# Kernel optimization log

Hardware: AMD Instinct MI355X
Metric: run time of the kernel (lower is better)

The kernel has to match this reference:

```python
import jax, jax.numpy as jnp
import numpy as np

B = 65536
IN = 64
H = 16
PF = 64


def _linear_params(key, out_dim, in_dim):
    k1, k2 = jax.random.split(key)
    bound = 1.0 / np.sqrt(in_dim)
    W = jax.random.uniform(k1, (out_dim, in_dim), jnp.float32, -bound, bound)
    b = jax.random.uniform(k2, (out_dim,), jnp.float32, -bound, bound)
    return W, b


def setup_inputs() -> dict:
    key = jax.random.key(0)
    ks = jax.random.split(key, 20)
    inp = {}
    for i, name in enumerate(['a', 'v', 'l', 'p_a', 'p_v', 'p_l', 'mean']):
        inp[name] = jax.random.normal(ks[i], (B, IN), jnp.float32)
    inp['Wa'], inp['ba'] = _linear_params(ks[7], H, IN)
    inp['Wv'], inp['bv'] = _linear_params(ks[8], H, IN)
    inp['Wl'], inp['bl'] = _linear_params(ks[9], H, IN)
    inp['Wap'], inp['bap'] = _linear_params(ks[10], H, IN)
    inp['Wvp'], inp['bvp'] = _linear_params(ks[11], H, IN)
    inp['Wlp'], inp['blp'] = _linear_params(ks[12], H, IN)
    inp['Wf1'], inp['bf1'] = _linear_params(ks[13], PF, H ** 3 // 16)
    inp['Wfp1'], inp['bfp1'] = _linear_params(ks[14], PF, H ** 3 // 16)
    inp['Wng'], inp['bng'] = _linear_params(ks[15], 64, 128)
    inp['rm1'] = jnp.zeros((128,), jnp.float32)  # normGate2 running_mean buffers (eval mode)
    inp['rm2'] = jnp.zeros((128,), jnp.float32)
    return inp


def _maxpool2(x):
    # 2x2 stride-2 max pool over the last two dims of [B, Hd, Wd]
    b, hd, wd = x.shape
    return x.reshape(b, hd // 2, 2, wd // 2, 2).max(axis=(2, 4))


def _trimodal_fusion(x_h, y_h, z_h):
    # outer product [B,H,H] -> pool -> [B,H*H//4,1] bmm [B,1,H] -> pool -> flatten
    f = x_h[:, :, None] * y_h[:, None, :]            # [B,16,16]
    f = _maxpool2(f)                                 # [B,8,8]
    f = f.reshape(-1, H * H // 4, 1) * z_h[:, None, :]  # [B,64,16]
    f = _maxpool2(f)                                 # [B,32,8]
    return f.reshape(x_h.shape[0], -1)               # [B,256]


def _norm_gate(x, running_mean):
    # eval-mode normGate2: y = x * sigmoid(|x - running_mean|)
    return x * jax.nn.sigmoid(jnp.abs(x - running_mean))


def reference(a, v, l, p_a, p_v, p_l, mean,
              Wa, ba, Wv, bv, Wl, bl, Wap, bap, Wvp, bvp, Wlp, blp,
              Wf1, bf1, Wfp1, bfp1, Wng, bng, rm1, rm2):
    a_h = jax.nn.sigmoid(a @ Wa.T + ba)
    v_h = jax.nn.sigmoid(v @ Wv.T + bv)
    l_h = jax.nn.sigmoid(l @ Wl.T + bl)
    fusion_1 = jax.nn.leaky_relu(_trimodal_fusion(a_h, v_h, l_h) @ Wf1.T + bf1)

    pa_h = jax.nn.sigmoid(p_a @ Wap.T + bap)
    pv_h = jax.nn.sigmoid(p_v @ Wvp.T + bvp)
    pl_h = jax.nn.sigmoid(p_l @ Wlp.T + blp)
    fusion_2 = jax.nn.leaky_relu(_trimodal_fusion(pa_h, pv_h, pl_h) @ Wfp1.T + bfp1)

    out = _norm_gate(jnp.concatenate([fusion_2, mean], axis=1), rm1)   # [B,128]
    out = out @ Wng.T + bng                                            # [B,64]
    out = _norm_gate(jnp.concatenate([out, fusion_1], axis=1), rm2)    # [B,128]
    return out
```

## Files before the change

### kernel.cpp

```cpp
#include <hip/hip_runtime.h>
#include <hip/hip_bf16.h>


typedef __attribute__((ext_vector_type(8))) short short8;
typedef __attribute__((ext_vector_type(4))) float f32x4;

#define MFMA16(A, B, C) __builtin_amdgcn_mfma_f32_16x16x32_bf16((A), (B), (C), 0, 0, 0)

__device__ __forceinline__ float fast_sigmoid(float x) {
    return __builtin_amdgcn_rcpf(1.0f + __expf(-x));
}
__device__ __forceinline__ float gate(float x, float rm) {
    return x * fast_sigmoid(fabsf(x - rm));
}
__device__ __forceinline__ float lrelu(float x) {
    return x >= 0.0f ? x : 0.01f * x;
}
__device__ __forceinline__ short f2bf(float f) {
    union { float f; unsigned u; } x; x.f = f;
    unsigned r = (x.u + 0x7FFF + ((x.u >> 16) & 1)) >> 16;
    return (short)r;
}
__device__ __forceinline__ short8 pack8(const float* xs) {
    union { short8 s; __hip_bfloat162 h[4]; } u;
    #pragma unroll
    for (int i = 0; i < 4; ++i) {
        float2 t; t.x = xs[2 * i]; t.y = xs[2 * i + 1];
        u.h[i] = __float22bfloat162_rn(t);
    }
    return u.s;
}
__device__ __forceinline__ f32x4 pmax_xor(f32x4 v, int mask) {
    f32x4 r;
    #pragma unroll
    for (int i = 0; i < 4; ++i) r[i] = fmaxf(v[i], __shfl_xor(v[i], mask, 64));
    return r;
}

__device__ __forceinline__ void proj_mfma2(const float* __restrict__ xbase,
                                           const short8* __restrict__ wfr,
                                           const float* __restrict__ bias,
                                           int lane, f32x4& h0, f32x4& h1) {
    const int m = lane & 15, quad = lane >> 4;
    f32x4 a0; a0[0] = a0[1] = a0[2] = a0[3] = 0.0f;
    f32x4 a1 = a0;
    #pragma unroll
    for (int t = 0; t < 2; ++t) {
        const float4* p0 = (const float4*)(xbase + m * 64 + t * 32 + quad * 8);
        const float4* p1 = (const float4*)(xbase + (16 + m) * 64 + t * 32 + quad * 8);
        float4 u0 = p0[0], u1 = p0[1];
        float4 w0 = p1[0], w1 = p1[1];
        const short8 frag = wfr[t * 64 + lane];
        float xs0[8] = {u0.x, u0.y, u0.z, u0.w, u1.x, u1.y, u1.z, u1.w};
        float xs1[8] = {w0.x, w0.y, w0.z, w0.w, w1.x, w1.y, w1.z, w1.w};
        a0 = MFMA16(pack8(xs0), frag, a0);
        a1 = MFMA16(pack8(xs1), frag, a1);
    }
    const float bn = bias[m];
    #pragma unroll
    for (int r = 0; r < 4; ++r) {
        h0[r] = fast_sigmoid(a0[r] + bn);
        h1[r] = fast_sigmoid(a1[r] + bn);
    }
}

__device__ __forceinline__ void stage_pools(f32x4 hx, f32x4 hy, f32x4 hz, int lane,
                                            float* __restrict__ sX,
                                            float* __restrict__ sY,
                                            float* __restrict__ sZ) {
    const int quad = lane >> 4, ln = lane & 15;
    f32x4 X = pmax_xor(hx, 1);
    f32x4 Y = pmax_xor(pmax_xor(hy, 1), 2);
    f32x4 Z = pmax_xor(hz, 1);
    #pragma unroll
    for (int r = 0; r < 4; ++r) {
        const int sm = quad * 4 + r;
        sX[(ln >> 1) * 16 + sm] = X[r];
        sY[(ln >> 2) * 16 + sm] = Y[r];
        sZ[(ln >> 1) * 16 + sm] = Z[r];
    }
}

__device__ __forceinline__ void fusion_mfma2(const short8* __restrict__ wfr,
                                             const float* __restrict__ bias,
                                             const float* __restrict__ sP0,
                                             const float* __restrict__ sP1,
                                             int lane,
                                             f32x4 acc0[4], f32x4 acc1[4]) {
    const int m = lane & 15, quad = lane >> 4;
    const float* sX0 = sP0;       const float* sY0 = sP0 + 128; const float* sZ0 = sP0 + 192;
    const float* sX1 = sP1;       const float* sY1 = sP1 + 128; const float* sZ1 = sP1 + 192;
    #pragma unroll
    for (int nt = 0; nt < 4; ++nt) {
        const float bb = bias[nt * 16 + m];
        acc0[nt][0] = acc0[nt][1] = acc0[nt][2] = acc0[nt][3] = bb;
        acc1[nt][0] = acc1[nt][1] = acc1[nt][2] = acc1[nt][3] = bb;
    }
    float zr0[8], zr1[8];
    #pragma unroll
    for (int j = 0; j < 8; ++j) { zr0[j] = sZ0[j * 16 + m]; zr1[j] = sZ1[j * 16 + m]; }
    const float yq0 = sY0[quad * 16 + m];
    const float yq1 = sY1[quad * 16 + m];
    #pragma unroll
    for (int t = 0; t < 8; ++t) {
        const float xy0 = sX0[t * 16 + m] * yq0;
        const float xy1 = sX1[t * 16 + m] * yq1;
        float p0[8], p1[8];
        #pragma unroll
        for (int j = 0; j < 8; ++j) { p0[j] = xy0 * zr0[j]; p1[j] = xy1 * zr1[j]; }
        const short8 af0 = pack8(p0);
        const short8 af1 = pack8(p1);
        #pragma unroll
        for (int nt = 0; nt < 4; ++nt) {
            const short8 frag = wfr[(t * 4 + nt) * 64 + lane];
            acc0[nt] = MFMA16(af0, frag, acc0[nt]);
            acc1[nt] = MFMA16(af1, frag, acc1[nt]);
        }
    }
}

__global__ __launch_bounds__(256, 4)
void fused_fwd(const float* __restrict__ a,  const float* __restrict__ v,
               const float* __restrict__ l,  const float* __restrict__ pa,
               const float* __restrict__ pv, const float* __restrict__ pl,
               const float* __restrict__ mean,
               const float* __restrict__ ba,  const float* __restrict__ bv_,
               const float* __restrict__ bl_, const float* __restrict__ bap,
               const float* __restrict__ bvp, const float* __restrict__ blp,
               const float* __restrict__ bf1, const float* __restrict__ bfp1,
               const float* __restrict__ bng,
               const float* __restrict__ rm1, const float* __restrict__ rm2,
               const short* __restrict__ ws, float* __restrict__ out) {
    __shared__ __align__(16) float sPool[4 * 2 * 320];
    __shared__ __align__(16) short sF2[2 * 2 * 1280];

    const int tid = threadIdx.x;
    const int lane = tid & 63;
    const int w = tid >> 6;
    const int m = lane & 15;
    const int quad = lane >> 4;
    const int wi = w & 1;
    const int srow0 = blockIdx.x * 64 + wi * 32;

    float* sP0 = sPool + w * 640;
    float* sP1 = sP0 + 320;

    const short8* projFr = (const short8*)ws;
    const short8* wfFr   = (const short8*)(ws + 6144);
    const short8* wfpFr  = (const short8*)(ws + 22528);
    const short8* wngFr  = (const short8*)(ws + 38912);

    if (w < 2) {
        {
            f32x4 hx0, hx1, hy0, hy1, hz0, hz1;
            proj_mfma2(pa + (size_t)srow0 * 64, projFr + 3 * 128, bap, lane, hx0, hx1);
            proj_mfma2(pv + (size_t)srow0 * 64, projFr + 4 * 128, bvp, lane, hy0, hy1);
            proj_mfma2(pl + (size_t)srow0 * 64, projFr + 5 * 128, blp, lane, hz0, hz1);
            stage_pools(hx0, hy0, hz0, lane, sP0, sP0 + 128, sP0 + 192);
            stage_pools(hx1, hy1, hz1, lane, sP1, sP1 + 128, sP1 + 192);
        }
        f32x4 f20[4], f21[4];
        fusion_mfma2(wfpFr, bfp1, sP0, sP1, lane, f20, f21);

        short* sF0 = sF2 + wi * 2560;
        short* sF1 = sF0 + 1280;
        #pragma unroll
        for (int nt = 0; nt < 4; ++nt) {
            const float r1 = rm1[nt * 16 + m];
            #pragma unroll
            for (int r = 0; r < 4; ++r) {
                sF0[(quad * 4 + r) * 80 + nt * 16 + m] = f2bf(gate(lrelu(f20[nt][r]), r1));
                sF1[(quad * 4 + r) * 80 + nt * 16 + m] = f2bf(gate(lrelu(f21[nt][r]), r1));
            }
        }

        f32x4 h0[4], h1[4];
        #pragma unroll
        for (int nt = 0; nt < 4; ++nt) {
            const float bb = bng[nt * 16 + m];
            h0[nt][0] = h0[nt][1] = h0[nt][2] = h0[nt][3] = bb;
            h1[nt][0] = h1[nt][1] = h1[nt][2] = h1[nt][3] = bb;
        }
        #pragma unroll
        for (int t = 0; t < 2; ++t) {
            const short8 af0 = *(const short8*)(sF0 + m * 80 + t * 32 + quad * 8);
            const short8 af1 = *(const short8*)(sF1 + m * 80 + t * 32 + quad * 8);
            #pragma unroll
            for (int nt = 0; nt < 4; ++nt) {
                const short8 frag = wngFr[(t * 4 + nt) * 64 + lane];
                h0[nt] = MFMA16(af0, frag, h0[nt]);
                h1[nt] = MFMA16(af1, frag, h1[nt]);
            }
        }
        #pragma unroll
        for (int t2 = 0; t2 < 2; ++t2) {
            const float4* rp = (const float4*)(rm1 + 64 + t2 * 32 + quad * 8);
            float4 r0 = rp[0], r1 = rp[1];
            const float4* mp0 = (const float4*)(mean + (size_t)(srow0 + m) * 64 + t2 * 32 + quad * 8);
            const float4* mp1 = (const float4*)(mean + (size_t)(srow0 + 16 + m) * 64 + t2 * 32 + quad * 8);
            float4 u0 = mp0[0], u1 = mp0[1];
            float4 w0 = mp1[0], w1 = mp1[1];
            float g0[8] = { gate(u0.x, r0.x), gate(u0.y, r0.y), gate(u0.z, r0.z), gate(u0.w, r0.w),
                            gate(u1.x, r1.x), gate(u1.y, r1.y), gate(u1.z, r1.z), gate(u1.w, r1.w) };
            float g1[8] = { gate(w0.x, r0.x), gate(w0.y, r0.y), gate(w0.z, r0.z), gate(w0.w, r0.w),
                            gate(w1.x, r1.x), gate(w1.y, r1.y), gate(w1.z, r1.z), gate(w1.w, r1.w) };
            const short8 af0 = pack8(g0);
            const short8 af1 = pack8(g1);
            #pragma unroll
            for (int nt = 0; nt < 4; ++nt) {
                const short8 frag = wngFr[((2 + t2) * 4 + nt) * 64 + lane];
                h0[nt] = MFMA16(af0, frag, h0[nt]);
                h1[nt] = MFMA16(af1, frag, h1[nt]);
            }
        }

        #pragma unroll
        for (int nt = 0; nt < 4; ++nt) {
            const float r2a = rm2[nt * 16 + m];
            #pragma unroll
            for (int r = 0; r < 4; ++r) {
                const size_t row0 = (size_t)(srow0 + quad * 4 + r) * 128;
                const size_t row1 = (size_t)(srow0 + 16 + quad * 4 + r) * 128;
                out[row0 + nt * 16 + m] = gate(h0[nt][r], r2a);
                out[row1 + nt * 16 + m] = gate(h1[nt][r], r2a);
            }
        }
    } else {
        {
            f32x4 hx0, hx1, hy0, hy1, hz0, hz1;
            proj_mfma2(a + (size_t)srow0 * 64, projFr + 0 * 128, ba, lane, hx0, hx1);
            proj_mfma2(v + (size_t)srow0 * 64, projFr + 1 * 128, bv_, lane, hy0, hy1);
            proj_mfma2(l + (size_t)srow0 * 64, projFr + 2 * 128, bl_, lane, hz0, hz1);
            stage_pools(hx0, hy0, hz0, lane, sP0, sP0 + 128, sP0 + 192);
            stage_pools(hx1, hy1, hz1, lane, sP1, sP1 + 128, sP1 + 192);
        }
        f32x4 f10[4], f11[4];
        fusion_mfma2(wfFr, bf1, sP0, sP1, lane, f10, f11);

        #pragma unroll
        for (int nt = 0; nt < 4; ++nt) {
            const float r2b = rm2[64 + nt * 16 + m];
            #pragma unroll
            for (int r = 0; r < 4; ++r) {
                const size_t row0 = (size_t)(srow0 + quad * 4 + r) * 128;
                const size_t row1 = (size_t)(srow0 + 16 + quad * 4 + r) * 128;
                out[row0 + 64 + nt * 16 + m] = gate(lrelu(f10[nt][r]), r2b);
                out[row1 + 64 + nt * 16 + m] = gate(lrelu(f11[nt][r]), r2b);
            }
        }
    }
}

__global__ void build_frags(const float* __restrict__ Wa,  const float* __restrict__ Wv,
                            const float* __restrict__ Wl,  const float* __restrict__ Wap,
                            const float* __restrict__ Wvp, const float* __restrict__ Wlp,
                            const float* __restrict__ Wf1, const float* __restrict__ Wfp1,
                            const float* __restrict__ Wng, short* __restrict__ ws) {
    const int i = blockIdx.x * 256 + threadIdx.x;
    if (i >= 47104) return;
    float val;
    if (i < 6144) {
        const float* W[6] = {Wa, Wv, Wl, Wap, Wvp, Wlp};
        const int mi = i >> 10, r = i & 1023;
        const int t = r >> 9, lane = (r >> 3) & 63, j = r & 7;
        val = W[mi][(lane & 15) * 64 + t * 32 + (lane >> 4) * 8 + j];
    } else if (i < 38912) {
        int r = i - 6144;
        const float* W = (r < 16384) ? Wf1 : Wfp1;
        r &= 16383;
        const int tn = r >> 9, lane = (r >> 3) & 63, j = r & 7;
        const int t = tn >> 2, nt = tn & 3;
        val = W[(nt * 16 + (lane & 15)) * 256 + t * 32 + (lane >> 4) * 8 + j];
    } else {
        const int r = i - 38912;
        const int tn = r >> 9, lane = (r >> 3) & 63, j = r & 7;
        const int t = tn >> 2, nt = tn & 3;
        val = Wng[(nt * 16 + (lane & 15)) * 128 + t * 32 + (lane >> 4) * 8 + j];
    }
    ws[i] = f2bf(val);
}

extern "C" void kernel_launch(void* const* d_in, const int* in_sizes, int n_in,
                              void* d_out, int out_size, void* d_ws, size_t ws_size,
                              hipStream_t stream) {
    const float* a    = (const float*)d_in[0];
    const float* v    = (const float*)d_in[1];
    const float* l    = (const float*)d_in[2];
    const float* pa   = (const float*)d_in[3];
    const float* pv   = (const float*)d_in[4];
    const float* pl   = (const float*)d_in[5];
    const float* mean = (const float*)d_in[6];
    const float* Wa   = (const float*)d_in[7];
    const float* ba   = (const float*)d_in[8];
    const float* Wv   = (const float*)d_in[9];
    const float* bv   = (const float*)d_in[10];
    const float* Wl   = (const float*)d_in[11];
    const float* bl   = (const float*)d_in[12];
    const float* Wap  = (const float*)d_in[13];
    const float* bap  = (const float*)d_in[14];
    const float* Wvp  = (const float*)d_in[15];
    const float* bvp  = (const float*)d_in[16];
    const float* Wlp  = (const float*)d_in[17];
    const float* blp  = (const float*)d_in[18];
    const float* Wf1  = (const float*)d_in[19];
    const float* bf1  = (const float*)d_in[20];
    const float* Wfp1 = (const float*)d_in[21];
    const float* bfp1 = (const float*)d_in[22];
    const float* Wng  = (const float*)d_in[23];
    const float* bng  = (const float*)d_in[24];
    const float* rm1  = (const float*)d_in[25];
    const float* rm2  = (const float*)d_in[26];

    short* ws = (short*)d_ws;

    build_frags<<<184, 256, 0, stream>>>(Wa, Wv, Wl, Wap, Wvp, Wlp,
                                         Wf1, Wfp1, Wng, ws);
    fused_fwd<<<1024, 256, 0, stream>>>(a, v, l, pa, pv, pl, mean,
                                        ba, bv, bl, bap, bvp, blp,
                                        bf1, bfp1, bng, rm1, rm2,
                                        ws, (float*)d_out);
}
```

Baseline: 39.88 us.

## Split paths per block, prefetch inputs into registers, stage weight fragments in LDS

Each block now handles one fusion path (primary or prime) for 128 rows, with all four waves on the same path, instead of mixing both paths across waves for 64 rows. All input and mean tiles are loaded into registers up front so the global loads are issued together, and the bf16 weight fragments the path needs are copied into shared memory once per block rather than read from global memory for every MFMA. Launch bounds drop from 4 to 2 blocks per SM to allow the larger register and LDS footprint. The trade is lower occupancy and extra LDS traffic in exchange for better memory-level parallelism and fragment reuse, and the two block types now do unequal amounts of work.

```diff
diff --git a/kernel.cpp b/kernel.cpp
--- a/kernel.cpp
+++ b/kernel.cpp
@@ -37,22 +37,20 @@
     return r;
 }
 
-__device__ __forceinline__ void proj_mfma2(const float* __restrict__ xbase,
-                                           const short8* __restrict__ wfr,
-                                           const float* __restrict__ bias,
-                                           int lane, f32x4& h0, f32x4& h1) {
-    const int m = lane & 15, quad = lane >> 4;
+__device__ __forceinline__ void proj_mfma2r(const float4* in,
+                                            const short* __restrict__ wfr,
+                                            const float* __restrict__ bias,
+                                            int lane, f32x4& h0, f32x4& h1) {
+    const int m = lane & 15;
     f32x4 a0; a0[0] = a0[1] = a0[2] = a0[3] = 0.0f;
     f32x4 a1 = a0;
     #pragma unroll
     for (int t = 0; t < 2; ++t) {
-        const float4* p0 = (const float4*)(xbase + m * 64 + t * 32 + quad * 8);
-        const float4* p1 = (const float4*)(xbase + (16 + m) * 64 + t * 32 + quad * 8);
-        float4 u0 = p0[0], u1 = p0[1];
-        float4 w0 = p1[0], w1 = p1[1];
-        const short8 frag = wfr[t * 64 + lane];
-        float xs0[8] = {u0.x, u0.y, u0.z, u0.w, u1.x, u1.y, u1.z, u1.w};
-        float xs1[8] = {w0.x, w0.y, w0.z, w0.w, w1.x, w1.y, w1.z, w1.w};
+        const short8 frag = *(const short8*)(wfr + (t * 64 + lane) * 8);
+        float xs0[8] = {in[2*t].x, in[2*t].y, in[2*t].z, in[2*t].w,
+                        in[2*t+1].x, in[2*t+1].y, in[2*t+1].z, in[2*t+1].w};
+        float xs1[8] = {in[4+2*t].x, in[4+2*t].y, in[4+2*t].z, in[4+2*t].w,
+                        in[4+2*t+1].x, in[4+2*t+1].y, in[4+2*t+1].z, in[4+2*t+1].w};
         a0 = MFMA16(pack8(xs0), frag, a0);
         a1 = MFMA16(pack8(xs1), frag, a1);
     }
@@ -81,15 +79,15 @@
     }
 }
 
-__device__ __forceinline__ void fusion_mfma2(const short8* __restrict__ wfr,
+__device__ __forceinline__ void fusion_mfma2(const short* __restrict__ wfr,
                                              const float* __restrict__ bias,
                                              const float* __restrict__ sP0,
                                              const float* __restrict__ sP1,
                                              int lane,
                                              f32x4 acc0[4], f32x4 acc1[4]) {
     const int m = lane & 15, quad = lane >> 4;
-    const float* sX0 = sP0;       const float* sY0 = sP0 + 128; const float* sZ0 = sP0 + 192;
-    const float* sX1 = sP1;       const float* sY1 = sP1 + 128; const float* sZ1 = sP1 + 192;
+    const float* sX0 = sP0; const float* sY0 = sP0 + 128; const float* sZ0 = sP0 + 192;
+    const float* sX1 = sP1; const float* sY1 = sP1 + 128; const float* sZ1 = sP1 + 192;
     #pragma unroll
     for (int nt = 0; nt < 4; ++nt) {
         const float bb = bias[nt * 16 + m];
@@ -112,14 +110,14 @@
         const short8 af1 = pack8(p1);
         #pragma unroll
         for (int nt = 0; nt < 4; ++nt) {
-            const short8 frag = wfr[(t * 4 + nt) * 64 + lane];
+            const short8 frag = *(const short8*)(wfr + ((t * 4 + nt) * 64 + lane) * 8);
             acc0[nt] = MFMA16(af0, frag, acc0[nt]);
             acc1[nt] = MFMA16(af1, frag, acc1[nt]);
         }
     }
 }
 
-__global__ __launch_bounds__(256, 4)
+__global__ __launch_bounds__(256, 2)
 void fused_fwd(const float* __restrict__ a,  const float* __restrict__ v,
                const float* __restrict__ l,  const float* __restrict__ pa,
                const float* __restrict__ pv, const float* __restrict__ pl,
@@ -131,39 +129,74 @@
                const float* __restrict__ bng,
                const float* __restrict__ rm1, const float* __restrict__ rm2,
                const short* __restrict__ ws, float* __restrict__ out) {
-    __shared__ __align__(16) float sPool[4 * 2 * 320];
-    __shared__ __align__(16) short sF2[2 * 2 * 1280];
+    __shared__ __align__(16) short sFrag[27648];
+    __shared__ __align__(16) float sScratch[4][1280];
 
     const int tid = threadIdx.x;
     const int lane = tid & 63;
     const int w = tid >> 6;
     const int m = lane & 15;
     const int quad = lane >> 4;
-    const int wi = w & 1;
-    const int srow0 = blockIdx.x * 64 + wi * 32;
-
-    float* sP0 = sPool + w * 640;
+    const int p1 = blockIdx.x & 1;
+    const int chunk = blockIdx.x >> 1;
+    const int srow0 = chunk * 128 + w * 32;
+
+    const float* x0 = (p1 ? a : pa) + (size_t)srow0 * 64;
+    const float* x1 = (p1 ? v : pv) + (size_t)srow0 * 64;
+    const float* x2 = (p1 ? l : pl) + (size_t)srow0 * 64;
+    float4 inA[8], inB[8], inC[8];
+    #pragma unroll
+    for (int i = 0; i < 8; ++i) {
+        const int tile = i >> 2, t = (i >> 1) & 1, hf = i & 1;
+        const size_t off = (size_t)(tile * 16 + m) * 64 + t * 32 + quad * 8 + hf * 4;
+        inA[i] = *(const float4*)(x0 + off);
+        inB[i] = *(const float4*)(x1 + off);
+        inC[i] = *(const float4*)(x2 + off);
+    }
+    float4 inM[8];
+    if (!p1) {
+        #pragma unroll
+        for (int i = 0; i < 8; ++i) {
+            const int tile = i >> 2, t2 = (i >> 1) & 1, hf = i & 1;
+            inM[i] = *(const float4*)(mean + (size_t)(srow0 + tile * 16 + m) * 64
+                                      + t2 * 32 + quad * 8 + hf * 4);
+        }
+    }
+
+    {
+        const short* srcA = ws + (p1 ? 0 : 3072);
+        const short* srcB = ws + (p1 ? 6144 : 22528);
+        const int nU = p1 ? 38 : 54;
+        for (int u = w; u < nU; u += 4) {
+            const short* src = (u < 6)  ? srcA + u * 512
+                             : (u < 38) ? srcB + (u - 6) * 512
+                                        : ws + 38912 + (u - 38) * 512;
+            *(short8*)(&sFrag[u * 512 + lane * 8]) = *(const short8*)(src + lane * 8);
+        }
+    }
+    __syncthreads();
+
+    float* sP0 = sScratch[w];
     float* sP1 = sP0 + 320;
-
-    const short8* projFr = (const short8*)ws;
-    const short8* wfFr   = (const short8*)(ws + 6144);
-    const short8* wfpFr  = (const short8*)(ws + 22528);
-    const short8* wngFr  = (const short8*)(ws + 38912);
-
-    if (w < 2) {
+    short* sF0 = (short*)sScratch[w];
+    short* sF1 = sF0 + 1280;
+
+    const short* projT = sFrag;
+    const short* fusT  = sFrag + 3072;
+    const short* ngT   = sFrag + 19456;
+
+    if (!p1) {
         {
             f32x4 hx0, hx1, hy0, hy1, hz0, hz1;
-            proj_mfma2(pa + (size_t)srow0 * 64, projFr + 3 * 128, bap, lane, hx0, hx1);
-            proj_mfma2(pv + (size_t)srow0 * 64, projFr + 4 * 128, bvp, lane, hy0, hy1);
-            proj_mfma2(pl + (size_t)srow0 * 64, projFr + 5 * 128, blp, lane, hz0, hz1);
+            proj_mfma2r(inA, projT + 0 * 1024, bap, lane, hx0, hx1);
+            proj_mfma2r(inB, projT + 1 * 1024, bvp, lane, hy0, hy1);
+            proj_mfma2r(inC, projT + 2 * 1024, blp, lane, hz0, hz1);
             stage_pools(hx0, hy0, hz0, lane, sP0, sP0 + 128, sP0 + 192);
             stage_pools(hx1, hy1, hz1, lane, sP1, sP1 + 128, sP1 + 192);
         }
         f32x4 f20[4], f21[4];
-        fusion_mfma2(wfpFr, bfp1, sP0, sP1, lane, f20, f21);
-
-        short* sF0 = sF2 + wi * 2560;
-        short* sF1 = sF0 + 1280;
+        fusion_mfma2(fusT, bfp1, sP0, sP1, lane, f20, f21);
+
         #pragma unroll
         for (int nt = 0; nt < 4; ++nt) {
             const float r1 = rm1[nt * 16 + m];
@@ -187,7 +220,7 @@
             const short8 af1 = *(const short8*)(sF1 + m * 80 + t * 32 + quad * 8);
             #pragma unroll
             for (int nt = 0; nt < 4; ++nt) {
-                const short8 frag = wngFr[(t * 4 + nt) * 64 + lane];
+                const short8 frag = *(const short8*)(ngT + ((t * 4 + nt) * 64 + lane) * 8);
                 h0[nt] = MFMA16(af0, frag, h0[nt]);
                 h1[nt] = MFMA16(af1, frag, h1[nt]);
             }
@@ -196,10 +229,8 @@
         for (int t2 = 0; t2 < 2; ++t2) {
             const float4* rp = (const float4*)(rm1 + 64 + t2 * 32 + quad * 8);
             float4 r0 = rp[0], r1 = rp[1];
-            const float4* mp0 = (const float4*)(mean + (size_t)(srow0 + m) * 64 + t2 * 32 + quad * 8);
-            const float4* mp1 = (const float4*)(mean + (size_t)(srow0 + 16 + m) * 64 + t2 * 32 + quad * 8);
-            float4 u0 = mp0[0], u1 = mp0[1];
-            float4 w0 = mp1[0], w1 = mp1[1];
+            float4 u0 = inM[2 * t2], u1 = inM[2 * t2 + 1];
+            float4 w0 = inM[4 + 2 * t2], w1 = inM[4 + 2 * t2 + 1];
             float g0[8] = { gate(u0.x, r0.x), gate(u0.y, r0.y), gate(u0.z, r0.z), gate(u0.w, r0.w),
                             gate(u1.x, r1.x), gate(u1.y, r1.y), gate(u1.z, r1.z), gate(u1.w, r1.w) };
             float g1[8] = { gate(w0.x, r0.x), gate(w0.y, r0.y), gate(w0.z, r0.z), gate(w0.w, r0.w),
@@ -208,7 +239,7 @@
             const short8 af1 = pack8(g1);
             #pragma unroll
             for (int nt = 0; nt < 4; ++nt) {
-                const short8 frag = wngFr[((2 + t2) * 4 + nt) * 64 + lane];
+                const short8 frag = *(const short8*)(ngT + (((2 + t2) * 4 + nt) * 64 + lane) * 8);
                 h0[nt] = MFMA16(af0, frag, h0[nt]);
                 h1[nt] = MFMA16(af1, frag, h1[nt]);
             }
@@ -228,14 +259,14 @@
     } else {
         {
             f32x4 hx0, hx1, hy0, hy1, hz0, hz1;
-            proj_mfma2(a + (size_t)srow0 * 64, projFr + 0 * 128, ba, lane, hx0, hx1);
-            proj_mfma2(v + (size_t)srow0 * 64, projFr + 1 * 128, bv_, lane, hy0, hy1);
-            proj_mfma2(l + (size_t)srow0 * 64, projFr + 2 * 128, bl_, lane, hz0, hz1);
+            proj_mfma2r(inA, projT + 0 * 1024, ba, lane, hx0, hx1);
+            proj_mfma2r(inB, projT + 1 * 1024, bv_, lane, hy0, hy1);
+            proj_mfma2r(inC, projT + 2 * 1024, bl_, lane, hz0, hz1);
             stage_pools(hx0, hy0, hz0, lane, sP0, sP0 + 128, sP0 + 192);
             stage_pools(hx1, hy1, hz1, lane, sP1, sP1 + 128, sP1 + 192);
         }
         f32x4 f10[4], f11[4];
-        fusion_mfma2(wfFr, bf1, sP0, sP1, lane, f10, f11);
+        fusion_mfma2(fusT, bf1, sP0, sP1, lane, f10, f11);
 
         #pragma unroll
         for (int nt = 0; nt < 4; ++nt) {
```

New measurement: 51.52 us. 29.2% more time.
